# Performance work log

Hardware: AMD Instinct MI355X
Metric: run time of the kernel (lower is better)

Reference implementation:

```python
import jax, jax.numpy as jnp
import numpy as np

N = 8192          # num_nodes
E = 262144        # num_edges = N * avg_degree(32)
K_SIGN = 1000.0   # ExactModel k
EPSILON = 5.0     # ExactModel epsilon


def setup_inputs() -> dict:
    key = jax.random.key(0)
    k1, k2, k3, k4 = jax.random.split(key, 4)
    src = jax.random.randint(k1, (E,), 0, N)
    dst = jax.random.randint(k2, (E,), 0, N)
    edge_index = jnp.stack([src, dst]).astype(jnp.int32)          # (2, E)
    # partition vector, elements in {1, ..., N}
    p = jax.random.randint(k3, (N,), 1, N + 1).astype(jnp.float32)  # (N,)
    x = jax.random.normal(k4, (N, 1), dtype=jnp.float32)            # node features
    return {"edge_index": edge_index, "p": p, "x": x}


def reference(edge_index, p, x):
    """infoco1 (segment logsumexp over edges with self-loops) followed by one
    refine step: pairwise difference matrix + CustomSignFunction tanh + row-sum."""
    n = p.shape[0]
    log_n = jnp.log(jnp.asarray(n, dtype=p.dtype))
    loops = jnp.arange(n, dtype=edge_index.dtype)
    src = jnp.concatenate([edge_index[0], loops])   # add_self_loops
    dst = jnp.concatenate([edge_index[1], loops])
    # contributions_log = log(p_i) + p_j * log(N)
    contrib = jnp.log(p[src]) + p[dst] * log_n      # (E + N,)
    # numerically stable segment log-sum-exp over incoming edges of each node
    mx = jax.ops.segment_max(contrib, dst, num_segments=n)              # scatter_max
    se = jax.ops.segment_sum(jnp.exp(contrib - mx[dst]), dst, num_segments=n)  # scatter_add
    S = mx + jnp.log(se) + jnp.dot(x[:, 0], p)      # infoco1: S_log + <x, p>
    # refine: all-pairs sign refinement, D_1 = tanh(k * (X - X^T) - eps)
    X = S[:, None]                                   # (N, 1)
    D1 = jnp.tanh(K_SIGN * (X - X.T) - EPSILON)      # (N, N)
    return D1.sum(axis=1)                            # (N,)
```

## Files before the change

kernel.cpp:

```cpp
#include <hip/hip_runtime.h>
#include <math.h>

#define K_SIGN 1000.0f
#define EPSILON 5.0f

#define D_HI ((EPSILON + 12.0f) / K_SIGN)
#define D_LO ((EPSILON - 12.0f) / K_SIGN)

#define NB_HIST 64


__global__ void __launch_bounds__(256) k_hist(
        const int* __restrict__ src, const int* __restrict__ dst,
        const float* __restrict__ p, const float* __restrict__ x,
        int* __restrict__ Hpriv, double* __restrict__ C,
        int* __restrict__ PFX, int* __restrict__ pos, int e, int n) {
    __shared__ int buf[8192];
    __shared__ int csum[256];
    __shared__ double dred[4];
    int tid = threadIdx.x;
    int b = blockIdx.x;

    int4* b4 = (int4*)buf;
    for (int i = tid; i < n / 4; i += 256) b4[i] = make_int4(0, 0, 0, 0);
    __syncthreads();

    if (b < NB_HIST) {
        int per = (e + NB_HIST - 1) / NB_HIST;
        int t0 = b * per;
        int t1 = min(t0 + per, e);
        for (int t = t0 + tid; t < t1; t += 256)
            atomicAdd(&buf[dst[t]], (int)p[src[t]]);
        __syncthreads();
        int4* o4 = (int4*)(Hpriv + b * n);
        for (int i = tid; i < n / 4; i += 256) o4[i] = b4[i];
        return;
    }

    double acc = 0.0;
    for (int i = tid; i < n; i += 256) {
        float pv = p[i];
        atomicAdd(&buf[(int)pv - 1], 1);
        acc += (double)x[i] * (double)pv;
    }
    for (int off = 32; off > 0; off >>= 1)
        acc += __shfl_down(acc, off, 64);
    if ((tid & 63) == 0) dred[tid >> 6] = acc;
    __syncthreads();
    if (tid == 0) *C = dred[0] + dred[1] + dred[2] + dred[3];

    int cw = n / 256;
    int base = tid * cw;
    int s = 0;
    for (int k = 0; k < cw; ++k) s += buf[base + k];
    csum[tid] = s;
    __syncthreads();
    for (int off = 1; off < 256; off <<= 1) {
        int v = (tid >= off) ? csum[tid - off] : 0;
        __syncthreads();
        csum[tid] += v;
        __syncthreads();
    }
    int run = (tid == 0) ? 0 : csum[tid - 1];
    for (int k = 0; k < cw; ++k) {
        int h = buf[base + k];
        PFX[base + k] = run;
        pos[base + k] = run;
        run += h;
    }
    if (tid == 0) PFX[n] = n;
}

__global__ void __launch_bounds__(256) k_merge(
        const int* __restrict__ Hpriv, const float* __restrict__ p,
        const double* __restrict__ C, float* __restrict__ S,
        int* __restrict__ pos, int* __restrict__ order, int n, float log_n) {
    int i = blockIdx.x * 256 + threadIdx.x;
    if (i >= n) return;
    float pv = p[i];
    int t = (int)pv;
#pragma unroll 8
    for (int b = 0; b < NB_HIST; ++b) t += Hpriv[b * n + i];
    S[i] = (logf((float)t) + pv * log_n) + (float)(*C);
    int r = atomicAdd(&pos[(int)pv - 1], 1);
    order[r] = i;
}

__global__ void __launch_bounds__(256) k_out(const float* __restrict__ S,
                                             const float* __restrict__ p,
                                             const int* __restrict__ PFX,
                                             const int* __restrict__ order,
                                             float* __restrict__ out, int n) {
    int i = blockIdx.x * 256 + threadIdx.x;
    if (i >= n) return;
    int pi = (int)p[i];
    int base = PFX[pi - 1];
    int g = PFX[pi] - base;
    float si = S[i];
    float acc = (float)(base - (n - base - g));
    for (int k = 0; k < g; ++k) {
        int j = order[base + k];
        float d = si - S[j];
        if (d > D_HI) acc += 1.0f;
        else if (d < D_LO) acc -= 1.0f;
        else acc += tanhf(fmaf(K_SIGN, d, -EPSILON));
    }
    out[i] = acc;
}

extern "C" void kernel_launch(void* const* d_in, const int* in_sizes, int n_in,
                              void* d_out, int out_size, void* d_ws, size_t ws_size,
                              hipStream_t stream) {
    const int* edge_index = (const int*)d_in[0];
    const float* p = (const float*)d_in[1];
    const float* x = (const float*)d_in[2];
    float* out = (float*)d_out;

    int e = in_sizes[0] / 2;
    int n = in_sizes[1];
    const int* src = edge_index;
    const int* dst = edge_index + e;

    double* C = (double*)d_ws;
    float* S = (float*)((char*)d_ws + 16);
    int* PFX = (int*)(S + n);
    int* pos = PFX + (n + 4);
    int* order = pos + n;
    int* Hpriv = order + n;

    float log_n = logf((float)n);

    k_hist<<<NB_HIST + 1, 256, 0, stream>>>(src, dst, p, x, Hpriv, C,
                                            PFX, pos, e, n);
    k_merge<<<n / 256, 256, 0, stream>>>(Hpriv, p, C, S, pos, order, n, log_n);
    k_out<<<n / 256, 256, 0, stream>>>(S, p, PFX, order, out, n);
}
```

Baseline: 86.50 us.

## Fuse histogram, merge and output kernels into one cooperative grid-synced kernel

```diff
diff --git a/kernel.cpp b/kernel.cpp
--- a/kernel.cpp
+++ b/kernel.cpp
@@ -1,5 +1,8 @@
 #include <hip/hip_runtime.h>
+#include <hip/hip_cooperative_groups.h>
 #include <math.h>
+
+namespace cg = cooperative_groups;
 
 #define K_SIGN 1000.0f
 #define EPSILON 5.0f
@@ -8,104 +11,118 @@
 #define D_LO ((EPSILON - 12.0f) / K_SIGN)
 
 #define NB_HIST 64
+#define NBLK 256
 
 
-__global__ void __launch_bounds__(256) k_hist(
+__global__ void __launch_bounds__(256) k_fused(
         const int* __restrict__ src, const int* __restrict__ dst,
         const float* __restrict__ p, const float* __restrict__ x,
         int* __restrict__ Hpriv, double* __restrict__ C,
-        int* __restrict__ PFX, int* __restrict__ pos, int e, int n) {
+        int* __restrict__ PFX, int* __restrict__ pos,
+        int* __restrict__ order, float* __restrict__ S,
+        float* __restrict__ out, int e, int n, float log_n) {
+    cg::grid_group grid = cg::this_grid();
     __shared__ int buf[8192];
     __shared__ int csum[256];
     __shared__ double dred[4];
     int tid = threadIdx.x;
     int b = blockIdx.x;
 
-    int4* b4 = (int4*)buf;
-    for (int i = tid; i < n / 4; i += 256) b4[i] = make_int4(0, 0, 0, 0);
-    __syncthreads();
+    if (b <= NB_HIST) {
+        int4* b4 = (int4*)buf;
+        for (int i = tid; i < n / 4; i += 256) b4[i] = make_int4(0, 0, 0, 0);
+        __syncthreads();
+        if (b < NB_HIST) {
+            int per = e / NB_HIST;
+            int t0 = b * per;
+            for (int t = t0 + tid * 4; t < t0 + per; t += 1024) {
+                int4 s4 = *(const int4*)(src + t);
+                int4 d4 = *(const int4*)(dst + t);
+                atomicAdd(&buf[d4.x], (int)p[s4.x]);
+                atomicAdd(&buf[d4.y], (int)p[s4.y]);
+                atomicAdd(&buf[d4.z], (int)p[s4.z]);
+                atomicAdd(&buf[d4.w], (int)p[s4.w]);
+            }
+            __syncthreads();
+            int4* o4 = (int4*)(Hpriv + b * n);
+            for (int i = tid; i < n / 4; i += 256) o4[i] = b4[i];
+        } else {
+            double acc = 0.0;
+            for (int i = tid; i < n; i += 256) {
+                float pv = p[i];
+                atomicAdd(&buf[(int)pv - 1], 1);
+                acc += (double)x[i] * (double)pv;
+            }
+            for (int off = 32; off > 0; off >>= 1)
+                acc += __shfl_down(acc, off, 64);
+            if ((tid & 63) == 0) dred[tid >> 6] = acc;
+            __syncthreads();
+            if (tid == 0) *C = dred[0] + dred[1] + dred[2] + dred[3];
+            int cw = n / 256;
+            int base = tid * cw;
+            int s = 0;
+            for (int k = 0; k < cw; ++k) s += buf[base + k];
+            csum[tid] = s;
+            __syncthreads();
+            for (int off = 1; off < 256; off <<= 1) {
+                int v = (tid >= off) ? csum[tid - off] : 0;
+                __syncthreads();
+                csum[tid] += v;
+                __syncthreads();
+            }
+            int run = (tid == 0) ? 0 : csum[tid - 1];
+            for (int k = 0; k < cw; ++k) {
+                int h = buf[base + k];
+                PFX[base + k] = run;
+                pos[base + k] = run;
+                run += h;
+            }
+            if (tid == 0) PFX[n] = n;
+        }
+    }
+    grid.sync();
 
-    if (b < NB_HIST) {
-        int per = (e + NB_HIST - 1) / NB_HIST;
-        int t0 = b * per;
-        int t1 = min(t0 + per, e);
-        for (int t = t0 + tid; t < t1; t += 256)
-            atomicAdd(&buf[dst[t]], (int)p[src[t]]);
+    {
+        int ii = tid & 31;
+        int bb = tid >> 5;
+        int i = b * 32 + ii;
+        int sum = 0;
+#pragma unroll
+        for (int k = 0; k < NB_HIST / 8; ++k)
+            sum += Hpriv[(bb * (NB_HIST / 8) + k) * n + i];
+        buf[bb * 32 + ii] = sum;
         __syncthreads();
-        int4* o4 = (int4*)(Hpriv + b * n);
-        for (int i = tid; i < n / 4; i += 256) o4[i] = b4[i];
-        return;
+        if (tid < 32) {
+            int i2 = b * 32 + tid;
+            float pv = p[i2];
+            int t = (int)pv;
+#pragma unroll
+            for (int q = 0; q < 8; ++q) t += buf[q * 32 + tid];
+            S[i2] = (logf((float)t) + pv * log_n) + (float)(*C);
+            int r = atomicAdd(&pos[(int)pv - 1], 1);
+            order[r] = i2;
+        }
     }
+    grid.sync();
 
-    double acc = 0.0;
-    for (int i = tid; i < n; i += 256) {
-        float pv = p[i];
-        atomicAdd(&buf[(int)pv - 1], 1);
-        acc += (double)x[i] * (double)pv;
+    {
+        int i = b * 256 + tid;
+        if (i < n) {
+            int pi = (int)p[i];
+            int base = PFX[pi - 1];
+            int g = PFX[pi] - base;
+            float si = S[i];
+            float acc = (float)(base - (n - base - g));
+            for (int k = 0; k < g; ++k) {
+                int j = order[base + k];
+                float d = si - S[j];
+                if (d > D_HI) acc += 1.0f;
+                else if (d < D_LO) acc -= 1.0f;
+                else acc += tanhf(fmaf(K_SIGN, d, -EPSILON));
+            }
+            out[i] = acc;
+        }
     }
-    for (int off = 32; off > 0; off >>= 1)
-        acc += __shfl_down(acc, off, 64);
-    if ((tid & 63) == 0) dred[tid >> 6] = acc;
-    __syncthreads();
-    if (tid == 0) *C = dred[0] + dred[1] + dred[2] + dred[3];
-
-    int cw = n / 256;
-    int base = tid * cw;
-    int s = 0;
-    for (int k = 0; k < cw; ++k) s += buf[base + k];
-    csum[tid] = s;
-    __syncthreads();
-    for (int off = 1; off < 256; off <<= 1) {
-        int v = (tid >= off) ? csum[tid - off] : 0;
-        __syncthreads();
-        csum[tid] += v;
-        __syncthreads();
-    }
-    int run = (tid == 0) ? 0 : csum[tid - 1];
-    for (int k = 0; k < cw; ++k) {
-        int h = buf[base + k];
-        PFX[base + k] = run;
-        pos[base + k] = run;
-        run += h;
-    }
-    if (tid == 0) PFX[n] = n;
-}
-
-__global__ void __launch_bounds__(256) k_merge(
-        const int* __restrict__ Hpriv, const float* __restrict__ p,
-        const double* __restrict__ C, float* __restrict__ S,
-        int* __restrict__ pos, int* __restrict__ order, int n, float log_n) {
-    int i = blockIdx.x * 256 + threadIdx.x;
-    if (i >= n) return;
-    float pv = p[i];
-    int t = (int)pv;
-#pragma unroll 8
-    for (int b = 0; b < NB_HIST; ++b) t += Hpriv[b * n + i];
-    S[i] = (logf((float)t) + pv * log_n) + (float)(*C);
-    int r = atomicAdd(&pos[(int)pv - 1], 1);
-    order[r] = i;
-}
-
-__global__ void __launch_bounds__(256) k_out(const float* __restrict__ S,
-                                             const float* __restrict__ p,
-                                             const int* __restrict__ PFX,
-                                             const int* __restrict__ order,
-                                             float* __restrict__ out, int n) {
-    int i = blockIdx.x * 256 + threadIdx.x;
-    if (i >= n) return;
-    int pi = (int)p[i];
-    int base = PFX[pi - 1];
-    int g = PFX[pi] - base;
-    float si = S[i];
-    float acc = (float)(base - (n - base - g));
-    for (int k = 0; k < g; ++k) {
-        int j = order[base + k];
-        float d = si - S[j];
-        if (d > D_HI) acc += 1.0f;
-        else if (d < D_LO) acc -= 1.0f;
-        else acc += tanhf(fmaf(K_SIGN, d, -EPSILON));
-    }
-    out[i] = acc;
 }
 
 extern "C" void kernel_launch(void* const* d_in, const int* in_sizes, int n_in,
@@ -130,8 +147,12 @@
 
     float log_n = logf((float)n);
 
-    k_hist<<<NB_HIST + 1, 256, 0, stream>>>(src, dst, p, x, Hpriv, C,
-                                            PFX, pos, e, n);
-    k_merge<<<n / 256, 256, 0, stream>>>(Hpriv, p, C, S, pos, order, n, log_n);
-    k_out<<<n / 256, 256, 0, stream>>>(S, p, PFX, order, out, n);
+    void* args[] = {
+        (void*)&src, (void*)&dst, (void*)&p, (void*)&x,
+        (void*)&Hpriv, (void*)&C, (void*)&PFX, (void*)&pos,
+        (void*)&order, (void*)&S, (void*)&out,
+        (void*)&e, (void*)&n, (void*)&log_n
+    };
+    hipLaunchCooperativeKernel((const void*)k_fused, dim3(NBLK), dim3(256),
+                               args, 0, stream);
 }
```

New measurement: 148.4 us. 71.5% more time.
